# Optimization experiments

Measured on AMD Instinct MI355X. Metric: run time of the kernel, lower is better.

The kernel has to match this reference:

```python
import jax, jax.numpy as jnp
import numpy as np

SEQ = 8192      # sequence_size
EMB = 64        # embedSize
NCLS = 2        # numClasses
NLEAF = 8192    # leaves of a perfect binary tree (13 levels)


def setup_inputs() -> dict:
    key = jax.random.key(0)
    ks = jax.random.split(key, 7)
    s = 0.02  # small init scale so 13 stacked relu-linears stay numerically sane
    return {
        "leaf_seqs": jax.random.normal(ks[0], (NLEAF, SEQ), jnp.float32),
        "emb_W": jax.random.normal(ks[1], (EMB, SEQ), jnp.float32) * s,
        "emb_b": jax.random.normal(ks[2], (EMB,), jnp.float32) * s,
        "W_W": jax.random.normal(ks[3], (EMB, 2 * EMB), jnp.float32) * s,
        "W_b": jax.random.normal(ks[4], (EMB,), jnp.float32) * s,
        "proj_W": jax.random.normal(ks[5], (NCLS, EMB), jnp.float32) * s,
        "proj_b": jax.random.normal(ks[6], (NCLS,), jnp.float32) * s,
    }


def reference(leaf_seqs, emb_W, emb_b, W_W, W_b, proj_W, proj_b):
    # Leaves: relu(embedding(seq)) for every leaf, batched. [NLEAF, EMB]
    h = jax.nn.relu(jnp.einsum('ns,es->ne', leaf_seqs, emb_W) + emb_b)
    # Internal nodes: combine adjacent sibling pairs level by level
    # (left-to-right recursion over a perfect binary tree == adjacent pairing).
    depth = int(np.log2(NLEAF))  # 13 levels, static Python loop
    for _ in range(depth):
        pair = jnp.concatenate([h[0::2], h[1::2]], axis=1)  # [N/2, 2*EMB]
        h = jax.nn.relu(jnp.einsum('nc,ec->ne', pair, W_W) + W_b)
    # Root: projection logits, [1, NCLS] (forward() only emits the root).
    return jnp.einsum('ne,ce->nc', h, proj_W) + proj_b
```

## Files before the change

kernel.cpp:

```cpp
#include <hip/hip_runtime.h>

#define SEQ   8192
#define EMB   64
#define NLEAF 8192
#define KQ    2048
#define KT    64
#define NT    (KQ / KT)

typedef __attribute__((ext_vector_type(4))) float        f32x4;
typedef __attribute__((ext_vector_type(4))) unsigned int u32x4;

__device__ __forceinline__ unsigned pack2(float x, float y) {
    return __builtin_amdgcn_perm(__float_as_uint(y), __float_as_uint(x), 0x07060302u);
}
__device__ __forceinline__ float bftrunc(float x) {
    return __uint_as_float(__float_as_uint(x) & 0xffff0000u);
}

__device__ __forceinline__ void mfma16(f32x4& d, const u32x4 a, const u32x4 b) {
    asm("v_mfma_f32_16x16x32_bf16 %0, %1, %2, %0" : "+v"(d) : "v"(a), "v"(b));
}

__device__ __forceinline__ void frag_cvt(const float* buf, int row, int kk,
                                         u32x4& hi, u32x4& lo) {
    const int c = kk >> 2;
    const int s = row & 7;
    const char* base = (const char*)buf + row * 256;
    const f32x4 v0 = *(const f32x4*)(base + 16 * (c ^ s));
    const f32x4 v1 = *(const f32x4*)(base + 16 * ((c + 1) ^ s));
    u32x4 h, l;
    h[0] = pack2(v0.x, v0.y);
    h[1] = pack2(v0.z, v0.w);
    h[2] = pack2(v1.x, v1.y);
    h[3] = pack2(v1.z, v1.w);
    l[0] = pack2(v0.x - bftrunc(v0.x), v0.y - bftrunc(v0.y));
    l[1] = pack2(v0.z - bftrunc(v0.z), v0.w - bftrunc(v0.w));
    l[2] = pack2(v1.x - bftrunc(v1.x), v1.y - bftrunc(v1.y));
    l[3] = pack2(v1.z - bftrunc(v1.z), v1.w - bftrunc(v1.w));
    hi = h; lo = l;
}

#define GLDS16(gp, lp) \
    __builtin_amdgcn_global_load_lds( \
        (const __attribute__((address_space(1))) void*)(gp), \
        (__attribute__((address_space(3))) void*)(lp), 16, 0, 0)

__global__ __launch_bounds__(256, 2) void k_gemm(
        const float* __restrict__ A, const float* __restrict__ W,
        float* __restrict__ P)
{
    __shared__ float sA[2][64 * 64];
    __shared__ float sW[2][64 * 64];

    const int tid  = threadIdx.x;
    const int lane = tid & 63;
    const int wid  = tid >> 6;

    const int g     = blockIdx.x >> 2;
    const int q     = blockIdx.x & 3;
    const int gl0   = g * 64;
    const int kbase = q * KQ;

    const int lr = lane >> 4;
    const int lc = lane & 15;

    const float* pA[4];
    const float* pW[4];
    #pragma unroll
    for (int j = 0; j < 4; ++j) {
        const int row = wid * 16 + j * 4 + lr;
        const int ch  = lc ^ ((j * 4 + lr) & 7);
        pA[j] = A + (size_t)(gl0 + row) * SEQ + kbase + ch * 4;
        pW[j] = W + (size_t)row * SEQ + kbase + ch * 4;
    }

    const int mt0 = (wid & 1) * 2;
    const int nt0 = (wid >> 1) * 2;
    const int fr  = lane & 15;
    const int fk  = (lane >> 4) * 8;

    f32x4 acc00 = {0.f, 0.f, 0.f, 0.f};
    f32x4 acc01 = {0.f, 0.f, 0.f, 0.f};
    f32x4 acc10 = {0.f, 0.f, 0.f, 0.f};
    f32x4 acc11 = {0.f, 0.f, 0.f, 0.f};

#define STAGE(bi_) do { \
    _Pragma("unroll") \
    for (int j = 0; j < 4; ++j) { \
        GLDS16(pA[j], &sA[bi_][(wid * 16 + j * 4) * 64]); \
        GLDS16(pW[j], &sW[bi_][(wid * 16 + j * 4) * 64]); \
        pA[j] += KT; pW[j] += KT; \
    } \
} while (0)

#define COMPUTE(bi_) do { \
    const float* bufA_ = &sA[bi_][0]; \
    const float* bufW_ = &sW[bi_][0]; \
    _Pragma("unroll") \
    for (int k32 = 0; k32 < 64; k32 += 32) { \
        u32x4 ah0, al0, ah1, al1, bh0, bl0, bh1, bl1; \
        frag_cvt(bufA_, mt0 * 16 + fr,      k32 + fk, ah0, al0); \
        frag_cvt(bufA_, mt0 * 16 + 16 + fr, k32 + fk, ah1, al1); \
        frag_cvt(bufW_, nt0 * 16 + fr,      k32 + fk, bh0, bl0); \
        frag_cvt(bufW_, nt0 * 16 + 16 + fr, k32 + fk, bh1, bl1); \
        mfma16(acc00, ah0, bh0); mfma16(acc00, ah0, bl0); mfma16(acc00, al0, bh0); \
        mfma16(acc01, ah0, bh1); mfma16(acc01, ah0, bl1); mfma16(acc01, al0, bh1); \
        mfma16(acc10, ah1, bh0); mfma16(acc10, ah1, bl0); mfma16(acc10, al1, bh0); \
        mfma16(acc11, ah1, bh1); mfma16(acc11, ah1, bl1); mfma16(acc11, al1, bh1); \
    } \
} while (0)

    STAGE(0);
    asm volatile("s_waitcnt vmcnt(0)" ::: "memory");
    __builtin_amdgcn_s_barrier();
    asm volatile("" ::: "memory");

    #pragma unroll 1
    for (int t = 0; t < NT; ++t) {
        const int p = t & 1;
        if (t + 1 < NT) {
            STAGE(p ^ 1);
            asm volatile("" ::: "memory");
        }
        COMPUTE(p);
        asm volatile("s_waitcnt vmcnt(0) lgkmcnt(0)" ::: "memory");
        __builtin_amdgcn_s_barrier();
        asm volatile("" ::: "memory");
    }

#undef STAGE
#undef COMPUTE

    float* Pq = P + (size_t)q * NLEAF * EMB;
    const int r0 = (lane >> 4) * 4;
    const int cn = lane & 15;
    #pragma unroll
    for (int r = 0; r < 4; ++r) {
        Pq[(size_t)(gl0 + (mt0 + 0) * 16 + r0 + r) * EMB + (nt0 + 0) * 16 + cn] = acc00[r];
        Pq[(size_t)(gl0 + (mt0 + 0) * 16 + r0 + r) * EMB + (nt0 + 1) * 16 + cn] = acc01[r];
        Pq[(size_t)(gl0 + (mt0 + 1) * 16 + r0 + r) * EMB + (nt0 + 0) * 16 + cn] = acc10[r];
        Pq[(size_t)(gl0 + (mt0 + 1) * 16 + r0 + r) * EMB + (nt0 + 1) * 16 + cn] = acc11[r];
    }
}

__device__ __forceinline__ void load_Wt(float (*Wt)[132],
                                        const float* __restrict__ WW, int tid) {
    const int e  = tid >> 2;
    const int c0 = (tid & 3) * 32;
    #pragma unroll
    for (int j = 0; j < 32; j += 4)
        *(f32x4*)&Wt[e][c0 + j] = *(const f32x4*)&WW[e * 128 + c0 + j];
}

__device__ __forceinline__ float hsum4(const f32x4 a) {
    return a.x + a.y + a.z + a.w;
}

__device__ __forceinline__ float* tree_levels(float* bufA, float* bufB,
        const float (*Wt)[132], float wb, int n0, int nlv, int tid)
{
    const int lane = tid & 63;
    const int wid  = tid >> 6;
    float* src = bufA;
    float* dst = bufB;
    int n = n0;
    for (int lvl = 0; lvl < nlv; ++lvl) {
        const int nodes = n >> 1;
        for (int base = wid * 4; base < nodes; base += 16) {
            const int cnt = (nodes - base < 4) ? (nodes - base) : 4;
            if (cnt == 4) {
                f32x4 ac0 = {0.f,0.f,0.f,0.f}, ac1 = ac0, ac2 = ac0, ac3 = ac0;
                const float* x0 = src + (2 * (base + 0)) * 68;
                const float* x1 = src + (2 * (base + 1)) * 68;
                const float* x2 = src + (2 * (base + 2)) * 68;
                const float* x3 = src + (2 * (base + 3)) * 68;
                #pragma unroll
                for (int j = 0; j < 32; ++j) {
                    const f32x4 w4 = *(const f32x4*)&Wt[lane][4 * j];
                    const int off = (j < 16) ? (4 * j) : (68 + 4 * (j - 16));
                    ac0 += w4 * *(const f32x4*)(x0 + off);
                    ac1 += w4 * *(const f32x4*)(x1 + off);
                    ac2 += w4 * *(const f32x4*)(x2 + off);
                    ac3 += w4 * *(const f32x4*)(x3 + off);
                }
                dst[(base + 0) * 68 + lane] = fmaxf(wb + hsum4(ac0), 0.f);
                dst[(base + 1) * 68 + lane] = fmaxf(wb + hsum4(ac1), 0.f);
                dst[(base + 2) * 68 + lane] = fmaxf(wb + hsum4(ac2), 0.f);
                dst[(base + 3) * 68 + lane] = fmaxf(wb + hsum4(ac3), 0.f);
            } else {
                for (int u = 0; u < cnt; ++u) {
                    f32x4 ac = {0.f, 0.f, 0.f, 0.f};
                    const float* x = src + (2 * (base + u)) * 68;
                    #pragma unroll
                    for (int j = 0; j < 32; ++j) {
                        const f32x4 w4 = *(const f32x4*)&Wt[lane][4 * j];
                        const int off = (j < 16) ? (4 * j) : (68 + 4 * (j - 16));
                        ac += w4 * *(const f32x4*)(x + off);
                    }
                    dst[(base + u) * 68 + lane] = fmaxf(wb + hsum4(ac), 0.f);
                }
            }
        }
        __syncthreads();
        float* tswp = src; src = dst; dst = tswp;
        n = nodes;
    }
    return src;
}

__global__ __launch_bounds__(256) void k_tree32(const float* __restrict__ P,
        const float* __restrict__ eb, const float* __restrict__ WW,
        const float* __restrict__ Wb, float* __restrict__ roots)
{
    __shared__ float hA[32][68];
    __shared__ float hB[16][68];
    __shared__ float Wt[64][132];
    const int tid = threadIdx.x;
    const int b   = blockIdx.x;
    load_Wt(Wt, WW, tid);
    {
        const int lf = tid >> 3;
        const int e0 = (tid & 7) * 8;
        const size_t base = (size_t)(b * 32 + lf) * EMB + e0;
        f32x4 s0 = *(const f32x4*)&P[base];
        f32x4 s1 = *(const f32x4*)&P[base + 4];
        s0 += *(const f32x4*)&P[(size_t)1 * NLEAF * EMB + base];
        s1 += *(const f32x4*)&P[(size_t)1 * NLEAF * EMB + base + 4];
        s0 += *(const f32x4*)&P[(size_t)2 * NLEAF * EMB + base];
        s1 += *(const f32x4*)&P[(size_t)2 * NLEAF * EMB + base + 4];
        s0 += *(const f32x4*)&P[(size_t)3 * NLEAF * EMB + base];
        s1 += *(const f32x4*)&P[(size_t)3 * NLEAF * EMB + base + 4];
        s0 += *(const f32x4*)&eb[e0];
        s1 += *(const f32x4*)&eb[e0 + 4];
        s0.x = fmaxf(s0.x, 0.f); s0.y = fmaxf(s0.y, 0.f);
        s0.z = fmaxf(s0.z, 0.f); s0.w = fmaxf(s0.w, 0.f);
        s1.x = fmaxf(s1.x, 0.f); s1.y = fmaxf(s1.y, 0.f);
        s1.z = fmaxf(s1.z, 0.f); s1.w = fmaxf(s1.w, 0.f);
        *(f32x4*)&hA[lf][e0]     = s0;
        *(f32x4*)&hA[lf][e0 + 4] = s1;
    }
    const float wb = Wb[tid & 63];
    __syncthreads();
    float* root = tree_levels(&hA[0][0], &hB[0][0], Wt, wb, 32, 5, tid);
    if (tid < 64) roots[b * 64 + tid] = root[tid];
}

__global__ __launch_bounds__(256) void k_tree16(const float* __restrict__ in,
        const float* __restrict__ WW, const float* __restrict__ Wb,
        float* __restrict__ outv)
{
    __shared__ float hA[32][68];
    __shared__ float hB[16][68];
    __shared__ float Wt[64][132];
    const int tid = threadIdx.x;
    load_Wt(Wt, WW, tid);
    {
        const int r  = tid >> 4;
        const int e0 = (tid & 15) * 4;
        *(f32x4*)&hA[r][e0] =
            *(const f32x4*)&in[(size_t)(blockIdx.x * 16 + r) * EMB + e0];
    }
    const float wb = Wb[tid & 63];
    __syncthreads();
    float* root = tree_levels(&hA[0][0], &hB[0][0], Wt, wb, 16, 4, tid);
    if (tid < 64) outv[blockIdx.x * 64 + tid] = root[tid];
}

__global__ __launch_bounds__(256) void k_root(const float* __restrict__ in,
        const float* __restrict__ WW, const float* __restrict__ Wb,
        const float* __restrict__ pW, const float* __restrict__ pb,
        float* __restrict__ out)
{
    __shared__ float hA[32][68];
    __shared__ float hB[16][68];
    __shared__ float Wt[64][132];
    const int tid = threadIdx.x;
    load_Wt(Wt, WW, tid);
    {
        const int r  = tid >> 4;
        const int e0 = (tid & 15) * 4;
        *(f32x4*)&hA[r][e0] = *(const f32x4*)&in[(size_t)r * EMB + e0];
    }
    const float wb = Wb[tid & 63];
    __syncthreads();
    float* root = tree_levels(&hA[0][0], &hB[0][0], Wt, wb, 16, 4, tid);
    if (tid < 64) {
        const float hv = root[tid];
        float t0 = hv * pW[tid];
        float t1 = hv * pW[64 + tid];
        #pragma unroll
        for (int off = 32; off > 0; off >>= 1) {
            t0 += __shfl_down(t0, off);
            t1 += __shfl_down(t1, off);
        }
        if (tid == 0) { out[0] = t0 + pb[0]; out[1] = t1 + pb[1]; }
    }
}

extern "C" void kernel_launch(void* const* d_in, const int* in_sizes, int n_in,
                              void* d_out, int out_size, void* d_ws, size_t ws_size,
                              hipStream_t stream)
{
    const float* A  = (const float*)d_in[0];
    const float* eW = (const float*)d_in[1];
    const float* eb = (const float*)d_in[2];
    const float* WW = (const float*)d_in[3];
    const float* Wb = (const float*)d_in[4];
    const float* pW = (const float*)d_in[5];
    const float* pb = (const float*)d_in[6];
    float* out = (float*)d_out;

    float* P     = (float*)d_ws;
    float* roots = P + (size_t)4 * NLEAF * EMB;
    float* l9    = roots + 256 * EMB;

    k_gemm  <<<dim3(512), dim3(256), 0, stream>>>(A, eW, P);
    k_tree32<<<dim3(256), dim3(256), 0, stream>>>(P, eb, WW, Wb, roots);
    k_tree16<<<dim3(16),  dim3(256), 0, stream>>>(roots, WW, Wb, l9);
    k_root  <<<dim3(1),   dim3(256), 0, stream>>>(l9, WW, Wb, pW, pb, out);
}
```

Baseline: 91.56 us.

## Use single-pass RNE bf16 GEMM with pre-tiled bf16 weights and triple buffering

Replaces the split hi/lo bf16 emulation (three MFMAs per tile) with a single round-to-nearest bf16 MFMA per tile. The embedding weights are converted once per call into a swizzled bf16 tile layout by a new kernel, which halves W load traffic and removes W conversion from the GEMM inner loop. The GEMM also moves from double to triple LDS buffering with a partial vmcnt wait, and each wave now owns 16 rows across all 64 columns. Dropping the lo correction lowers accuracy to plain bf16 on a K=8192 reduction, and the extra conversion kernel adds a launch.

Measured after the change: 82.58 us (median of 2 runs). 9.8% less time.

```diff
diff --git a/kernel.cpp b/kernel.cpp
--- a/kernel.cpp
+++ b/kernel.cpp
@@ -10,34 +10,29 @@
 typedef __attribute__((ext_vector_type(4))) float        f32x4;
 typedef __attribute__((ext_vector_type(4))) unsigned int u32x4;
 
-__device__ __forceinline__ unsigned pack2(float x, float y) {
-    return __builtin_amdgcn_perm(__float_as_uint(y), __float_as_uint(x), 0x07060302u);
-}
-__device__ __forceinline__ float bftrunc(float x) {
-    return __uint_as_float(__float_as_uint(x) & 0xffff0000u);
+__device__ __forceinline__ unsigned rne_pair(float x, float y) {
+    const unsigned ux = __float_as_uint(x), uy = __float_as_uint(y);
+    const unsigned rx = (ux + 0x7fffu + ((ux >> 16) & 1u)) >> 16;
+    const unsigned ry = (uy + 0x7fffu + ((uy >> 16) & 1u)) & 0xffff0000u;
+    return rx | ry;
 }
 
 __device__ __forceinline__ void mfma16(f32x4& d, const u32x4 a, const u32x4 b) {
     asm("v_mfma_f32_16x16x32_bf16 %0, %1, %2, %0" : "+v"(d) : "v"(a), "v"(b));
 }
 
-__device__ __forceinline__ void frag_cvt(const float* buf, int row, int kk,
-                                         u32x4& hi, u32x4& lo) {
+__device__ __forceinline__ u32x4 frag_rne(const float* buf, int row, int kk) {
     const int c = kk >> 2;
     const int s = row & 7;
     const char* base = (const char*)buf + row * 256;
     const f32x4 v0 = *(const f32x4*)(base + 16 * (c ^ s));
     const f32x4 v1 = *(const f32x4*)(base + 16 * ((c + 1) ^ s));
-    u32x4 h, l;
-    h[0] = pack2(v0.x, v0.y);
-    h[1] = pack2(v0.z, v0.w);
-    h[2] = pack2(v1.x, v1.y);
-    h[3] = pack2(v1.z, v1.w);
-    l[0] = pack2(v0.x - bftrunc(v0.x), v0.y - bftrunc(v0.y));
-    l[1] = pack2(v0.z - bftrunc(v0.z), v0.w - bftrunc(v0.w));
-    l[2] = pack2(v1.x - bftrunc(v1.x), v1.y - bftrunc(v1.y));
-    l[3] = pack2(v1.z - bftrunc(v1.z), v1.w - bftrunc(v1.w));
-    hi = h; lo = l;
+    u32x4 h;
+    h[0] = rne_pair(v0.x, v0.y);
+    h[1] = rne_pair(v0.z, v0.w);
+    h[2] = rne_pair(v1.x, v1.y);
+    h[3] = rne_pair(v1.z, v1.w);
+    return h;
 }
 
 #define GLDS16(gp, lp) \
@@ -45,12 +40,33 @@
         (const __attribute__((address_space(1))) void*)(gp), \
         (__attribute__((address_space(3))) void*)(lp), 16, 0, 0)
 
+__global__ __launch_bounds__(256) void k_cvtW(const float* __restrict__ W,
+                                              unsigned* __restrict__ Wt)
+{
+    const int gid  = blockIdx.x * 256 + threadIdx.x;
+    const int chsw = gid & 7;
+    const int row  = (gid >> 3) & 63;
+    const int t    = (gid >> 9) & 31;
+    const int q    = gid >> 14;
+    const int c    = chsw ^ (row & 7);
+    const float* src = W + (size_t)row * SEQ + q * KQ + t * KT + c * 8;
+    const f32x4 a = *(const f32x4*)(src);
+    const f32x4 b = *(const f32x4*)(src + 4);
+    u32x4 v;
+    v[0] = rne_pair(a.x, a.y);
+    v[1] = rne_pair(a.z, a.w);
+    v[2] = rne_pair(b.x, b.y);
+    v[3] = rne_pair(b.z, b.w);
+    u32x4* dst = (u32x4*)(Wt + ((q * 32 + t) * 512 + row * 8 + chsw) * 4);
+    *dst = v;
+}
+
 __global__ __launch_bounds__(256, 2) void k_gemm(
-        const float* __restrict__ A, const float* __restrict__ W,
+        const float* __restrict__ A, const char* __restrict__ Wt,
         float* __restrict__ P)
 {
-    __shared__ float sA[2][64 * 64];
-    __shared__ float sW[2][64 * 64];
+    __shared__ float sA[3][64 * 64];
+    __shared__ char  sW[3][8192];
 
     const int tid  = threadIdx.x;
     const int lane = tid & 63;
@@ -64,82 +80,86 @@
     const int lr = lane >> 4;
     const int lc = lane & 15;
 
-    const float* pA[4];
-    const float* pW[4];
-    #pragma unroll
-    for (int j = 0; j < 4; ++j) {
-        const int row = wid * 16 + j * 4 + lr;
-        const int ch  = lc ^ ((j * 4 + lr) & 7);
-        pA[j] = A + (size_t)(gl0 + row) * SEQ + kbase + ch * 4;
-        pW[j] = W + (size_t)row * SEQ + kbase + ch * 4;
-    }
-
-    const int mt0 = (wid & 1) * 2;
-    const int nt0 = (wid >> 1) * 2;
-    const int fr  = lane & 15;
-    const int fk  = (lane >> 4) * 8;
-
-    f32x4 acc00 = {0.f, 0.f, 0.f, 0.f};
-    f32x4 acc01 = {0.f, 0.f, 0.f, 0.f};
-    f32x4 acc10 = {0.f, 0.f, 0.f, 0.f};
-    f32x4 acc11 = {0.f, 0.f, 0.f, 0.f};
+    const float* pA0;
+    const float* pA1;
+    const float* pA2;
+    const float* pA3;
+    {
+        const int r0 = wid * 16 + 0 * 4 + lr;
+        const int r1 = wid * 16 + 1 * 4 + lr;
+        const int r2 = wid * 16 + 2 * 4 + lr;
+        const int r3 = wid * 16 + 3 * 4 + lr;
+        pA0 = A + (size_t)(gl0 + r0) * SEQ + kbase + (lc ^ (r0 & 7)) * 4;
+        pA1 = A + (size_t)(gl0 + r1) * SEQ + kbase + (lc ^ (r1 & 7)) * 4;
+        pA2 = A + (size_t)(gl0 + r2) * SEQ + kbase + (lc ^ (r2 & 7)) * 4;
+        pA3 = A + (size_t)(gl0 + r3) * SEQ + kbase + (lc ^ (r3 & 7)) * 4;
+    }
+    const char* pW = Wt + (size_t)(q * 32) * 8192 + (2 * wid) * 1024 + lane * 16;
+
+    const int fr = lane & 15;
+    const int fq = lane >> 4;
+
+    f32x4 acc0 = {0.f, 0.f, 0.f, 0.f};
+    f32x4 acc1 = {0.f, 0.f, 0.f, 0.f};
+    f32x4 acc2 = {0.f, 0.f, 0.f, 0.f};
+    f32x4 acc3 = {0.f, 0.f, 0.f, 0.f};
 
 #define STAGE(bi_) do { \
+    char* wdst = (char*)&sW[bi_][0] + 2 * wid * 1024; \
+    GLDS16(pW, wdst); \
+    GLDS16(pW + 1024, wdst + 1024); \
+    pW += 8192; \
+    GLDS16(pA0, &sA[bi_][(wid * 16 + 0) * 64]); \
+    GLDS16(pA1, &sA[bi_][(wid * 16 + 4) * 64]); \
+    GLDS16(pA2, &sA[bi_][(wid * 16 + 8) * 64]); \
+    GLDS16(pA3, &sA[bi_][(wid * 16 + 12) * 64]); \
+    pA0 += KT; pA1 += KT; pA2 += KT; pA3 += KT; \
+} while (0)
+
+#define COMPUTE(bi_) do { \
+    const float* bufA_ = &sA[bi_][0]; \
+    const char*  bufW_ = &sW[bi_][0]; \
     _Pragma("unroll") \
-    for (int j = 0; j < 4; ++j) { \
-        GLDS16(pA[j], &sA[bi_][(wid * 16 + j * 4) * 64]); \
-        GLDS16(pW[j], &sW[bi_][(wid * 16 + j * 4) * 64]); \
-        pA[j] += KT; pW[j] += KT; \
+    for (int k32 = 0; k32 < 2; ++k32) { \
+        const u32x4 af = frag_rne(bufA_, wid * 16 + fr, k32 * 32 + fq * 8); \
+        const int baddr = fr * 128 + 16 * ((k32 * 4 + fq) ^ (fr & 7)); \
+        const u32x4 b0 = *(const u32x4*)(bufW_ + baddr); \
+        const u32x4 b1 = *(const u32x4*)(bufW_ + 2048 + baddr); \
+        const u32x4 b2 = *(const u32x4*)(bufW_ + 4096 + baddr); \
+        const u32x4 b3 = *(const u32x4*)(bufW_ + 6144 + baddr); \
+        mfma16(acc0, af, b0); \
+        mfma16(acc1, af, b1); \
+        mfma16(acc2, af, b2); \
+        mfma16(acc3, af, b3); \
     } \
 } while (0)
 
-#define COMPUTE(bi_) do { \
-    const float* bufA_ = &sA[bi_][0]; \
-    const float* bufW_ = &sW[bi_][0]; \
-    _Pragma("unroll") \
-    for (int k32 = 0; k32 < 64; k32 += 32) { \
-        u32x4 ah0, al0, ah1, al1, bh0, bl0, bh1, bl1; \
-        frag_cvt(bufA_, mt0 * 16 + fr,      k32 + fk, ah0, al0); \
-        frag_cvt(bufA_, mt0 * 16 + 16 + fr, k32 + fk, ah1, al1); \
-        frag_cvt(bufW_, nt0 * 16 + fr,      k32 + fk, bh0, bl0); \
-        frag_cvt(bufW_, nt0 * 16 + 16 + fr, k32 + fk, bh1, bl1); \
-        mfma16(acc00, ah0, bh0); mfma16(acc00, ah0, bl0); mfma16(acc00, al0, bh0); \
-        mfma16(acc01, ah0, bh1); mfma16(acc01, ah0, bl1); mfma16(acc01, al0, bh1); \
-        mfma16(acc10, ah1, bh0); mfma16(acc10, ah1, bl0); mfma16(acc10, al1, bh0); \
-        mfma16(acc11, ah1, bh1); mfma16(acc11, ah1, bl1); mfma16(acc11, al1, bh1); \
-    } \
-} while (0)
-
     STAGE(0);
-    asm volatile("s_waitcnt vmcnt(0)" ::: "memory");
-    __builtin_amdgcn_s_barrier();
-    asm volatile("" ::: "memory");
-
+    STAGE(1);
+
+    int bcur = 0, bnxt = 1, bfut = 2;
     #pragma unroll 1
     for (int t = 0; t < NT; ++t) {
-        const int p = t & 1;
-        if (t + 1 < NT) {
-            STAGE(p ^ 1);
-            asm volatile("" ::: "memory");
-        }
-        COMPUTE(p);
-        asm volatile("s_waitcnt vmcnt(0) lgkmcnt(0)" ::: "memory");
+        if (t + 1 < NT) asm volatile("s_waitcnt vmcnt(6)" ::: "memory");
+        else            asm volatile("s_waitcnt vmcnt(0)" ::: "memory");
         __builtin_amdgcn_s_barrier();
-        asm volatile("" ::: "memory");
+        __builtin_amdgcn_sched_barrier(0);
+        if (t + 2 < NT) STAGE(bfut);
+        COMPUTE(bcur);
+        const int tmp = bcur; bcur = bnxt; bnxt = bfut; bfut = tmp;
     }
 
 #undef STAGE
 #undef COMPUTE
 
     float* Pq = P + (size_t)q * NLEAF * EMB;
-    const int r0 = (lane >> 4) * 4;
-    const int cn = lane & 15;
+    const int row0 = gl0 + wid * 16 + fq * 4;
     #pragma unroll
     for (int r = 0; r < 4; ++r) {
-        Pq[(size_t)(gl0 + (mt0 + 0) * 16 + r0 + r) * EMB + (nt0 + 0) * 16 + cn] = acc00[r];
-        Pq[(size_t)(gl0 + (mt0 + 0) * 16 + r0 + r) * EMB + (nt0 + 1) * 16 + cn] = acc01[r];
-        Pq[(size_t)(gl0 + (mt0 + 1) * 16 + r0 + r) * EMB + (nt0 + 0) * 16 + cn] = acc10[r];
-        Pq[(size_t)(gl0 + (mt0 + 1) * 16 + r0 + r) * EMB + (nt0 + 1) * 16 + cn] = acc11[r];
+        Pq[(size_t)(row0 + r) * EMB +  0 + fr] = acc0[r];
+        Pq[(size_t)(row0 + r) * EMB + 16 + fr] = acc1[r];
+        Pq[(size_t)(row0 + r) * EMB + 32 + fr] = acc2[r];
+        Pq[(size_t)(row0 + r) * EMB + 48 + fr] = acc3[r];
     }
 }
 
@@ -313,8 +333,10 @@
     float* P     = (float*)d_ws;
     float* roots = P + (size_t)4 * NLEAF * EMB;
     float* l9    = roots + 256 * EMB;
-
-    k_gemm  <<<dim3(512), dim3(256), 0, stream>>>(A, eW, P);
+    char*  Wtil  = (char*)d_ws + (size_t)16 * 1024 * 1024;
+
+    k_cvtW  <<<dim3(256), dim3(256), 0, stream>>>(eW, (unsigned*)Wtil);
+    k_gemm  <<<dim3(512), dim3(256), 0, stream>>>(A, Wtil, P);
     k_tree32<<<dim3(256), dim3(256), 0, stream>>>(P, eb, WW, Wb, roots);
     k_tree16<<<dim3(16),  dim3(256), 0, stream>>>(roots, WW, Wb, l9);
     k_root  <<<dim3(1),   dim3(256), 0, stream>>>(l9, WW, Wb, pW, pb, out);
```
